# Kernel tuning notes

Hardware: AMD Instinct MI355X
Metric: run time of the kernel (lower is better)

Reference implementation:

```python
import jax, jax.numpy as jnp
import numpy as np

B, N, DIM, H = 2, 2048, 1024, 16
D = DIM // H  # head_dim = 64


def setup_inputs() -> dict:
    key = jax.random.key(0)
    ks = jax.random.split(key, 3)
    w_scale = 0.02
    return {
        "x": jax.random.normal(ks[0], (B, N, DIM), dtype=jnp.float32),
        "Wqkv": jax.random.normal(ks[1], (DIM, 3 * DIM), dtype=jnp.float32) * w_scale,
        "bqkv": jnp.zeros((3 * DIM,), dtype=jnp.float32),
        "Wproj": jax.random.normal(ks[2], (DIM, DIM), dtype=jnp.float32) * w_scale,
        "bproj": jnp.zeros((DIM,), dtype=jnp.float32),
        "sigma": jnp.ones((1,), dtype=jnp.float32),
        "gamma": jnp.ones((1,), dtype=jnp.float32),
    }


def reference(x, Wqkv, bqkv, Wproj, bproj, sigma, gamma):
    b, n, c = x.shape
    # qkv projection -> (B, N, 3, H, D)
    qkv = (x @ Wqkv + bqkv).reshape(b, n, 3, H, D)
    q = jnp.transpose(qkv[:, :, 0], (0, 2, 1, 3))  # [B, H, N, D]
    k = jnp.transpose(qkv[:, :, 1], (0, 2, 1, 3))
    v = jnp.transpose(qkv[:, :, 2], (0, 2, 1, 3))
    scale = 1.0 / jnp.sqrt(jnp.asarray(D, dtype=x.dtype))
    scores = jnp.einsum("bhqd,bhkd->bhqk", q, k) * scale  # [B, H, N, N]
    # divisive normalization (cortical gain control) over key axis
    denom = sigma + jnp.sqrt(jnp.mean(scores * scores, axis=-1, keepdims=True))
    scores = gamma * scores / denom
    attn = jax.nn.softmax(scores, axis=-1)
    out = jnp.einsum("bhqk,bhkd->bhqd", attn, v)  # [B, H, N, D]
    out = jnp.transpose(out, (0, 2, 1, 3)).reshape(b, n, c)
    return out @ Wproj + bproj
```

## Files before the change

kernel.cpp:

```cpp
#include <hip/hip_runtime.h>

typedef __attribute__((ext_vector_type(4))) float f32x4;
typedef __attribute__((ext_vector_type(8))) _Float16 f16x8;
typedef __attribute__((ext_vector_type(4))) _Float16 f16x4;
typedef __attribute__((ext_vector_type(2))) _Float16 f16x2;

#define MFMA_F16(a, b, c) __builtin_amdgcn_mfma_f32_16x16x32_f16(a, b, c, 0, 0, 0)

__device__ __forceinline__ void gload_lds16(const void* g, void* l) {
  __builtin_amdgcn_global_load_lds(
      (const __attribute__((address_space(1))) void*)g,
      (__attribute__((address_space(3))) void*)l, 16, 0, 0);
}
__device__ __forceinline__ f16x2 pk2(float a, float b) {
  return __builtin_bit_cast(f16x2, __builtin_amdgcn_cvt_pkrtz(a, b));
}
__device__ __forceinline__ void pipe_barrier_v4() {
  asm volatile("s_waitcnt vmcnt(4) lgkmcnt(0)" ::: "memory");
  __builtin_amdgcn_sched_barrier(0);
  __builtin_amdgcn_s_barrier();
}
__device__ __forceinline__ void pipe_barrier_v3() {
  asm volatile("s_waitcnt vmcnt(3) lgkmcnt(0)" ::: "memory");
  __builtin_amdgcn_sched_barrier(0);
  __builtin_amdgcn_s_barrier();
}
__device__ __forceinline__ void pipe_barrier_v2() {
  asm volatile("s_waitcnt vmcnt(2) lgkmcnt(0)" ::: "memory");
  __builtin_amdgcn_sched_barrier(0);
  __builtin_amdgcn_s_barrier();
}
__device__ __forceinline__ void pipe_barrier_v0() {
  asm volatile("s_waitcnt vmcnt(0) lgkmcnt(0)" ::: "memory");
  __builtin_amdgcn_sched_barrier(0);
  __builtin_amdgcn_s_barrier();
}

__global__ __launch_bounds__(256) void prep_kernel(
    const float* __restrict__ x, _Float16* __restrict__ xf,
    const float* __restrict__ Wqkv, _Float16* __restrict__ wqt,
    const float* __restrict__ Wproj, _Float16* __restrict__ wpt) {
  __shared__ float tile[32][33];
  const int bx = blockIdx.x;
  if (bx < 4096) {
    const int i = bx * 256 + threadIdx.x;
    f32x4 v = *(const f32x4*)(x + (size_t)i * 4);
    f16x4 h;
#pragma unroll
    for (int j = 0; j < 4; ++j) h[j] = (_Float16)v[j];
    *(f16x4*)(xf + (size_t)i * 4) = h;
    return;
  }
  const float* W;
  _Float16* wt;
  int N, n0, k0;
  if (bx < 7168) {
    const int t = bx - 4096;
    W = Wqkv; wt = wqt; N = 3072;
    n0 = (t % 96) * 32; k0 = (t / 96) * 32;
  } else {
    const int t = bx - 7168;
    W = Wproj; wt = wpt; N = 1024;
    n0 = (t % 32) * 32; k0 = (t / 32) * 32;
  }
  const int tx = threadIdx.x & 31, ty = threadIdx.x >> 5;
#pragma unroll
  for (int j = 0; j < 32; j += 8)
    tile[ty + j][tx] = W[(size_t)(k0 + ty + j) * N + n0 + tx];
  __syncthreads();
#pragma unroll
  for (int j = 0; j < 32; j += 8)
    wt[(size_t)(n0 + ty + j) * 1024 + k0 + tx] = (_Float16)tile[tx][ty + j];
}

__global__ __launch_bounds__(256) void gemm_qkv_kernel(
    const _Float16* __restrict__ xf, const _Float16* __restrict__ wt,
    const float* __restrict__ bias, _Float16* __restrict__ QF,
    _Float16* __restrict__ KF, _Float16* __restrict__ KT,
    _Float16* __restrict__ VT) {
  __shared__ __attribute__((aligned(16))) _Float16 lg[24576];
  const int tid = threadIdx.x, lane = tid & 63, w = tid >> 6;
  const int wg = blockIdx.x;
  const int cx = wg & 7, c = wg >> 3;
  const int bxl = (cx & 1) * 12 + c % 12;
  const int byl = (cx >> 1) * 8 + c / 12;
  const int m0 = byl * 128, n0 = bxl * 128;
  const int wr = (w >> 1) * 64, wc = (w & 1) * 64;
  f32x4 acc[4][4] = {};

  const int srow = lane >> 2;
  const int scol = (((lane & 3) ^ ((lane >> 3) & 3)) * 8);
  const int fr = lane & 15, fg = lane >> 4;
  const int rswz = (fr >> 1) & 3;

  auto stageT = [&](int buf, int k0) {
#pragma unroll
    for (int j = 0; j < 2; ++j) {
      const int rbase = 32 * w + 16 * j;
      const int r = rbase + srow;
      gload_lds16(xf + (size_t)(m0 + r) * 1024 + k0 + scol,
                  &lg[buf * 8192 + rbase * 32]);
      gload_lds16(wt + (size_t)(n0 + r) * 1024 + k0 + scol,
                  &lg[buf * 8192 + 4096 + rbase * 32]);
    }
  };
  auto mfma_step = [&](int ab) {
    f16x8 af[4], bfr[4];
#pragma unroll
    for (int m = 0; m < 4; ++m)
      af[m] = *(const f16x8*)&lg[ab + (wr + 16 * m + fr) * 32 + ((fg ^ rswz) * 8)];
#pragma unroll
    for (int n = 0; n < 4; ++n)
      bfr[n] = *(const f16x8*)&lg[ab + 4096 + (wc + 16 * n + fr) * 32 + ((fg ^ rswz) * 8)];
#pragma unroll
    for (int m = 0; m < 4; ++m)
#pragma unroll
      for (int n = 0; n < 4; ++n) acc[m][n] = MFMA_F16(af[m], bfr[n], acc[m][n]);
  };

  stageT(0, 0);
  stageT(1, 32);
  pipe_barrier_v4();
  for (int T = 0; T < 30; T += 3) {
#pragma unroll
    for (int s = 0; s < 3; ++s) {
      stageT((s + 2) % 3, (T + s + 2) * 32);
      mfma_step(s * 8192);
      pipe_barrier_v4();
    }
  }
  mfma_step(0);
  pipe_barrier_v0();
  mfma_step(8192);
  pipe_barrier_v0();

  const int fq = fg * 4;
#pragma unroll
  for (int n = 0; n < 4; ++n) {
    const float bv = bias[n0 + wc + 16 * n + fr];
#pragma unroll
    for (int m = 0; m < 4; ++m)
#pragma unroll
      for (int i = 0; i < 4; ++i)
        lg[(wr + 16 * m + fq + i) * 129 + wc + 16 * n + fr] =
            (_Float16)(acc[m][n][i] + bv);
  }
  __syncthreads();
  const int b = m0 >> 11, nnb = m0 & 2047;
  const int h0 = 2 * (bxl & 7);
  const int sPhase = bxl >> 3;
  if (sPhase <= 1) {
    _Float16* __restrict__ dst = (sPhase == 0) ? QF : KF;
#pragma unroll
    for (int p = 0; p < 8; ++p) {
      const int r = p * 16 + (tid >> 4);
      const int cc = tid & 15;
      f16x8 vals;
#pragma unroll
      for (int j = 0; j < 8; ++j) vals[j] = lg[r * 129 + cc * 8 + j];
      const int h = cc >> 3, d = (cc & 7) * 8;
      *(f16x8*)&dst[((size_t)((b * 16 + h0 + h) * 2048 + nnb + r)) * 64 + d] = vals;
    }
  }
  if (sPhase >= 1) {
    _Float16* __restrict__ T = (sPhase == 1) ? KT : VT;
#pragma unroll
    for (int p = 0; p < 8; ++p) {
      const int lr = p * 16 + (tid >> 4);
      const int cc = tid & 15;
      f16x8 vals;
#pragma unroll
      for (int j = 0; j < 8; ++j) vals[j] = lg[(cc * 8 + j) * 129 + lr];
      const int h = lr >> 6, d = lr & 63;
      *(f16x8*)&T[((size_t)((b * 16 + h0 + h) * 64 + d)) * 2048 + nnb + cc * 8] = vals;
    }
  }
}

__global__ __launch_bounds__(256) void gram_partial_kernel(
    const _Float16* __restrict__ KT, float* __restrict__ GP) {
  __shared__ __attribute__((aligned(16))) _Float16 sT[3][4096];
  const int tid = threadIdx.x, lane = tid & 63, w = tid >> 6;
  const int bh = blockIdx.x >> 2, qt = blockIdx.x & 3;
  const _Float16* src = KT + (size_t)bh * 64 * 2048 + qt * 512;
  const int s_r = lane >> 3, s_cg = lane & 7;
  const int fr = lane & 15, fg = lane >> 4;
  const int kswz = fr & 7;

  auto stage = [&](int buf, int n0) {
#pragma unroll
    for (int j = 0; j < 2; ++j) {
      const int rbase = 8 * w + 32 * j;
      gload_lds16(src + (size_t)(rbase + s_r) * 2048 + n0 + ((s_cg ^ s_r) * 8),
                  &sT[buf][rbase * 64]);
    }
  };

  f32x4 acc[4] = {};
  stage(0, 0);
  stage(1, 64);
  pipe_barrier_v2();
  int cur = 0;
#pragma unroll
  for (int t = 0; t < 8; ++t) {
    if (t < 6) {
      const int nb = (cur + 2 >= 3) ? cur - 1 : cur + 2;
      stage(nb, (t + 2) * 64);
    }
    f16x8 af[2];
#pragma unroll
    for (int ks = 0; ks < 2; ++ks)
      af[ks] = *(const f16x8*)&sT[cur][(16 * w + fr) * 64 + (((ks * 4 + fg) ^ kswz) * 8)];
#pragma unroll
    for (int nt = 0; nt < 4; ++nt)
#pragma unroll
      for (int ks = 0; ks < 2; ++ks)
        acc[nt] = MFMA_F16(
            af[ks],
            *(const f16x8*)&sT[cur][(16 * nt + fr) * 64 + (((ks * 4 + fg) ^ kswz) * 8)],
            acc[nt]);
    if (t < 6) pipe_barrier_v2(); else pipe_barrier_v0();
    cur = (cur + 1 == 3) ? 0 : cur + 1;
  }
  float* dst = GP + (size_t)blockIdx.x * 4096;
#pragma unroll
  for (int nt = 0; nt < 4; ++nt)
#pragma unroll
    for (int i = 0; i < 4; ++i)
      dst[(16 * w + fg * 4 + i) * 64 + 16 * nt + fr] = acc[nt][i];
}

__global__ __launch_bounds__(256) void gram_reduce_kernel(
    const float* __restrict__ GP, _Float16* __restrict__ GH,
    _Float16* __restrict__ GL) {
  const int bh = blockIdx.x >> 2, seg = blockIdx.x & 3;
  const int e0 = seg * 1024 + threadIdx.x * 4;
  const float* p = GP + (size_t)bh * 4 * 4096 + e0;
  f32x4 s = *(const f32x4*)p;
  s += *(const f32x4*)(p + 4096);
  s += *(const f32x4*)(p + 8192);
  s += *(const f32x4*)(p + 12288);
  f16x4 gh, gl;
#pragma unroll
  for (int j = 0; j < 4; ++j) {
    gh[j] = (_Float16)s[j];
    gl[j] = (_Float16)(s[j] - (float)gh[j]);
  }
  *(f16x4*)&GH[(size_t)bh * 4096 + e0] = gh;
  *(f16x4*)&GL[(size_t)bh * 4096 + e0] = gl;
}

__global__ __launch_bounds__(256) void attn_kernel(
    const _Float16* __restrict__ QF, const _Float16* __restrict__ KF,
    const _Float16* __restrict__ VT, const _Float16* __restrict__ GH,
    const _Float16* __restrict__ GL, _Float16* __restrict__ OB,
    const float* __restrict__ sigma_p, const float* __restrict__ gamma_p) {
  __shared__ __attribute__((aligned(16))) _Float16 lds[32768];

  const int tid = threadIdx.x, lane = tid & 63, w = tid >> 6;
  const int wg = blockIdx.x;
  const int c = wg >> 3;
  const int bh = (wg & 7) * 4 + (c >> 4);
  const int q0 = (c & 15) * 128;
  const size_t base = (size_t)bh * (2048 * 64);
  const float sigma = sigma_p[0], gamma = gamma_p[0];
  const int fr = lane & 15, fg = lane >> 4;
  const int s_r = lane >> 3, s_cg = lane & 7;
  const int kswz = fr & 7;

  const _Float16* Kbh = KF + base;
  const _Float16* Tbh = VT + base;

  f16x8 qf[2][2];
#pragma unroll
  for (int m = 0; m < 2; ++m)
#pragma unroll
    for (int ks = 0; ks < 2; ++ks)
      qf[m][ks] = *(const f16x8*)(QF + base +
                                  (size_t)(q0 + 32 * w + 16 * m + fr) * 64 +
                                  ks * 32 + fg * 8);

  auto stage64 = [&](int dstoff, const _Float16* g, int srcstride) {
#pragma unroll
    for (int j = 0; j < 2; ++j) {
      const int rbase = 8 * w + 32 * j;
      gload_lds16(g + (size_t)(rbase + s_r) * srcstride + ((s_cg ^ s_r) * 8),
                  &lds[dstoff + rbase * 64]);
    }
  };
  auto stage64K = [&](int dstoff, const _Float16* g) {
#pragma unroll
    for (int j = 0; j < 2; ++j) {
      const int rbase = 8 * w + 32 * j;
      const int r = rbase + s_r;
      const int pr = (r & 0x23) | ((r & 0x0C) << 1) | ((r & 0x10) >> 2);
      gload_lds16(g + (size_t)pr * 64 + ((s_cg ^ s_r) * 8),
                  &lds[dstoff + rbase * 64]);
    }
  };
  auto stage_tile = [&](int b, int kb) {
    stage64K(b * 4096, Kbh + (size_t)kb * 4096);
    stage64(16384 + b * 4096, Tbh + kb * 64, 2048);
  };

  stage64(0, GH + (size_t)bh * 4096, 64);
  stage64(4096, GL + (size_t)bh * 4096, 64);
  __syncthreads();
  float minvl2[2];
  float* Yp = (float*)&lds[8192 + w * 2048];
#pragma unroll
  for (int m = 0; m < 2; ++m) {
    f32x4 yacc[4] = {};
#pragma unroll
    for (int nt = 0; nt < 4; ++nt) {
#pragma unroll
      for (int ks = 0; ks < 2; ++ks) {
        const int off = (16 * nt + fr) * 64 + (((ks * 4 + fg) ^ kswz) * 8);
        yacc[nt] = MFMA_F16(qf[m][ks], *(const f16x8*)&lds[off], yacc[nt]);
        yacc[nt] = MFMA_F16(qf[m][ks], *(const f16x8*)&lds[4096 + off], yacc[nt]);
      }
    }
#pragma unroll
    for (int nt = 0; nt < 4; ++nt)
#pragma unroll
      for (int i = 0; i < 4; ++i) Yp[(fg * 4 + i) * 64 + 16 * nt + fr] = yacc[nt][i];
    float zp = 0.0f;
#pragma unroll
    for (int ks = 0; ks < 2; ++ks) {
      const f32x4 y0 = *(const f32x4*)&Yp[fr * 64 + ks * 32 + fg * 8];
      const f32x4 y1 = *(const f32x4*)&Yp[fr * 64 + ks * 32 + fg * 8 + 4];
#pragma unroll
      for (int cc = 0; cc < 4; ++cc) {
        zp += y0[cc] * (float)qf[m][ks][cc];
        zp += y1[cc] * (float)qf[m][ks][cc + 4];
      }
    }
    zp += __shfl_xor(zp, 16);
    zp += __shfl_xor(zp, 32);
    const float rms = sqrtf(fmaxf(zp, 0.0f)) * (1.0f / 362.038672f);
    minvl2[m] = gamma / (sigma + rms) * 0.125f * 1.44269504f;
  }
#pragma unroll
  for (int m = 0; m < 2; ++m)
#pragma unroll
    for (int ks = 0; ks < 2; ++ks) {
      f16x8 q = qf[m][ks], r;
#pragma unroll
      for (int j = 0; j < 4; ++j) {
        const f16x2 t = pk2((float)q[2 * j] * minvl2[m],
                            (float)q[2 * j + 1] * minvl2[m]);
        r[2 * j] = t[0];
        r[2 * j + 1] = t[1];
      }
      qf[m][ks] = r;
    }
  __syncthreads();

  f32x4 oacc[2][4] = {};
  f32x4 lacc[2] = {};
  f16x8 ones;
#pragma unroll
  for (int j = 0; j < 8; ++j) ones[j] = (_Float16)1.0f;

  auto qk_tile = [&](int kbuf, f32x4 (&pn)[2][4]) {
#pragma unroll
    for (int n = 0; n < 4; ++n) {
      const int offb = kbuf * 4096 + (16 * n + fr) * 64;
      const f16x8 kf0 = *(const f16x8*)&lds[offb + ((fg ^ kswz) * 8)];
      const f16x8 kf1 = *(const f16x8*)&lds[offb + (((4 + fg) ^ kswz) * 8)];
#pragma unroll
      for (int m = 0; m < 2; ++m) {
        f32x4 a = {};
        a = MFMA_F16(kf0, qf[m][0], a);
        a = MFMA_F16(kf1, qf[m][1], a);
        pn[m][n] = a;
      }
    }
  };
  auto exp_pack = [&](f32x4 (&pn)[2][4], f16x8 (&pa)[2][2]) {
#pragma unroll
    for (int m = 0; m < 2; ++m) {
#pragma unroll
      for (int n = 0; n < 4; ++n)
#pragma unroll
        for (int i = 0; i < 4; ++i)
          pn[m][n][i] = __builtin_amdgcn_exp2f(pn[m][n][i]);
#pragma unroll
      for (int k2 = 0; k2 < 2; ++k2) {
        const f16x2 c0 = pk2(pn[m][2 * k2][0], pn[m][2 * k2][1]);
        const f16x2 c1 = pk2(pn[m][2 * k2][2], pn[m][2 * k2][3]);
        const f16x2 c2 = pk2(pn[m][2 * k2 + 1][0], pn[m][2 * k2 + 1][1]);
        const f16x2 c3 = pk2(pn[m][2 * k2 + 1][2], pn[m][2 * k2 + 1][3]);
        pa[m][k2][0] = c0[0]; pa[m][k2][1] = c0[1];
        pa[m][k2][2] = c1[0]; pa[m][k2][3] = c1[1];
        pa[m][k2][4] = c2[0]; pa[m][k2][5] = c2[1];
        pa[m][k2][6] = c3[0]; pa[m][k2][7] = c3[1];
      }
    }
  };
  auto pv_tile = [&](int vbuf, f16x8 (&pa)[2][2]) {
#pragma unroll
    for (int k2 = 0; k2 < 2; ++k2) {
#pragma unroll
      for (int nf = 0; nf < 4; ++nf) {
        const int off = 16384 + vbuf * 4096 + (16 * nf + fr) * 64 +
                        (((k2 * 4 + fg) ^ kswz) * 8);
        const f16x8 vt = *(const f16x8*)&lds[off];
        oacc[0][nf] = MFMA_F16(vt, pa[0][k2], oacc[0][nf]);
        oacc[1][nf] = MFMA_F16(vt, pa[1][k2], oacc[1][nf]);
      }
      lacc[0] = MFMA_F16(ones, pa[0][k2], lacc[0]);
      lacc[1] = MFMA_F16(ones, pa[1][k2], lacc[1]);
    }
  };

  f32x4 pn[2][4];
  f16x8 pa[2][2][2];

  stage_tile(0, 0);
  stage_tile(1, 1);
  stage_tile(2, 2);
  pipe_barrier_v4();
  qk_tile(0, pn);
  exp_pack(pn, pa[0]);

  for (int T = 0; T < 28; T += 4) {
#pragma unroll
    for (int s = 0; s < 4; ++s) {
      stage_tile((s + 3) & 3, T + s + 3);
      __builtin_amdgcn_s_setprio(1);
      qk_tile((s + 1) & 3, pn);
      __builtin_amdgcn_s_setprio(0);
      __builtin_amdgcn_s_setprio(1);
      pv_tile(s & 3, pa[s & 1]);
      __builtin_amdgcn_s_setprio(0);
      exp_pack(pn, pa[(s + 1) & 1]);
      pipe_barrier_v4();
    }
  }
  {
    stage_tile(3, 31);
    __builtin_amdgcn_s_setprio(1); qk_tile(1, pn); __builtin_amdgcn_s_setprio(0);
    __builtin_amdgcn_s_setprio(1); pv_tile(0, pa[0]); __builtin_amdgcn_s_setprio(0);
    exp_pack(pn, pa[1]);
    pipe_barrier_v4();
    __builtin_amdgcn_s_setprio(1); qk_tile(2, pn); __builtin_amdgcn_s_setprio(0);
    __builtin_amdgcn_s_setprio(1); pv_tile(1, pa[1]); __builtin_amdgcn_s_setprio(0);
    exp_pack(pn, pa[0]);
    pipe_barrier_v0();
    __builtin_amdgcn_s_setprio(1); qk_tile(3, pn); __builtin_amdgcn_s_setprio(0);
    __builtin_amdgcn_s_setprio(1); pv_tile(2, pa[0]); __builtin_amdgcn_s_setprio(0);
    exp_pack(pn, pa[1]);
    pipe_barrier_v0();
    __builtin_amdgcn_s_setprio(1); pv_tile(3, pa[1]); __builtin_amdgcn_s_setprio(0);
  }

  float inv[2];
#pragma unroll
  for (int m = 0; m < 2; ++m) inv[m] = 1.0f / lacc[m][0];

  const int b = bh >> 4, h = bh & 15;
#pragma unroll
  for (int m = 0; m < 2; ++m) {
    const size_t orow = (size_t)(b * 2048 + q0 + 32 * w + 16 * m + fr);
#pragma unroll
    for (int nf = 0; nf < 4; ++nf) {
      f16x4 ov;
#pragma unroll
      for (int i = 0; i < 4; ++i) ov[i] = (_Float16)(oacc[m][nf][i] * inv[m]);
      *(f16x4*)&OB[orow * 1024 + h * 64 + 16 * nf + 4 * fg] = ov;
    }
  }
}

__global__ __launch_bounds__(256) void gemm_proj_kernel(
    const _Float16* __restrict__ A, const _Float16* __restrict__ Bt,
    const float* __restrict__ bias, float* __restrict__ out) {
  __shared__ __attribute__((aligned(16))) _Float16 lg[18432];
  const int tid = threadIdx.x, lane = tid & 63, w = tid >> 6;
  const int wg = blockIdx.x;
  const int c = wg >> 3;
  const int bxl = c & 7;
  const int byl = (wg & 7) * 8 + (c >> 3);
  const int m0 = byl * 64, n0 = bxl * 128;
  const int wr = (w >> 1) * 32, wc = (w & 1) * 64;
  f32x4 acc[2][4] = {};
  const int srow = lane >> 2;
  const int scol = (((lane & 3) ^ ((lane >> 3) & 3)) * 8);
  const int fr = lane & 15, fg = lane >> 4;
  const int rswz = (fr >> 1) & 3;

  auto stageT = [&](int buf, int k0) {
    {
      const int rbase = 16 * w;
      gload_lds16(A + (size_t)(m0 + rbase + srow) * 1024 + k0 + scol,
                  &lg[buf * 6144 + rbase * 32]);
    }
#pragma unroll
    for (int j = 0; j < 2; ++j) {
      const int rbase = 32 * w + 16 * j;
      gload_lds16(Bt + (size_t)(n0 + rbase + srow) * 1024 + k0 + scol,
                  &lg[buf * 6144 + 2048 + rbase * 32]);
    }
  };
  auto mfma_step = [&](int ab) {
    f16x8 af[2], bfr[4];
#pragma unroll
    for (int m = 0; m < 2; ++m)
      af[m] = *(const f16x8*)&lg[ab + (wr + 16 * m + fr) * 32 + ((fg ^ rswz) * 8)];
#pragma unroll
    for (int n = 0; n < 4; ++n)
      bfr[n] = *(const f16x8*)&lg[ab + 2048 + (wc + 16 * n + fr) * 32 + ((fg ^ rswz) * 8)];
#pragma unroll
    for (int m = 0; m < 2; ++m)
#pragma unroll
      for (int n = 0; n < 4; ++n) acc[m][n] = MFMA_F16(af[m], bfr[n], acc[m][n]);
  };

  stageT(0, 0);
  stageT(1, 32);
  pipe_barrier_v3();
  for (int T = 0; T < 30; T += 3) {
#pragma unroll
    for (int s = 0; s < 3; ++s) {
      stageT((s + 2) % 3, (T + s + 2) * 32);
      mfma_step(s * 6144);
      pipe_barrier_v3();
    }
  }
  mfma_step(0);
  pipe_barrier_v0();
  mfma_step(6144);
  pipe_barrier_v0();

  const int fq = fg * 4;
#pragma unroll
  for (int n = 0; n < 4; ++n) {
    const int col = n0 + wc + 16 * n + fr;
    const float bv = bias[col];
#pragma unroll
    for (int m = 0; m < 2; ++m) {
#pragma unroll
      for (int i = 0; i < 4; ++i) {
        const int row = m0 + wr + 16 * m + fq + i;
        out[(size_t)row * 1024 + col] = acc[m][n][i] + bv;
      }
    }
  }
}

extern "C" void kernel_launch(void* const* d_in, const int* in_sizes, int n_in,
                              void* d_out, int out_size, void* d_ws, size_t ws_size,
                              hipStream_t stream) {
  const float* x = (const float*)d_in[0];
  const float* Wqkv = (const float*)d_in[1];
  const float* bqkv = (const float*)d_in[2];
  const float* Wproj = (const float*)d_in[3];
  const float* bproj = (const float*)d_in[4];
  const float* sigma = (const float*)d_in[5];
  const float* gamma = (const float*)d_in[6];
  float* out = (float*)d_out;

  char* ws = (char*)d_ws;
  const size_t MB = 1024 * 1024;
  _Float16* XF  = (_Float16*)(ws + 0 * MB);
  _Float16* WQT = (_Float16*)(ws + 8 * MB);
  _Float16* WPT = (_Float16*)(ws + 14 * MB);
  _Float16* QF  = (_Float16*)(ws + 16 * MB);
  _Float16* KF  = (_Float16*)(ws + 24 * MB);
  _Float16* VT  = (_Float16*)(ws + 32 * MB);
  _Float16* KT  = (_Float16*)(ws + 40 * MB);
  _Float16* OB  = (_Float16*)(ws + 40 * MB);
  _Float16* GH  = (_Float16*)(ws + 8 * MB);
  _Float16* GL  = (_Float16*)(ws + 8 * MB + 512 * 1024);
  float*    GP  = (float*)(ws + 9 * MB);

  prep_kernel<<<8192, 256, 0, stream>>>(x, XF, Wqkv, WQT, Wproj, WPT);
  gemm_qkv_kernel<<<768, 256, 0, stream>>>(XF, WQT, bqkv, QF, KF, KT, VT);
  gram_partial_kernel<<<128, 256, 0, stream>>>(KT, GP);
  gram_reduce_kernel<<<128, 256, 0, stream>>>(GP, GH, GL);
  attn_kernel<<<512, 256, 0, stream>>>(QF, KF, VT, GH, GL, OB, sigma, gamma);
  gemm_proj_kernel<<<512, 256, 0, stream>>>(OB, WPT, bproj, out);
}
```

Measured before the change: 115.9 us.

## Fuse x fp16 conversion into QKV GEMM loads and split Gram partials finer

Removes the separate x-to-fp16 conversion pass: the QKV GEMM now loads fp32 x tiles into registers, converts them and writes them to LDS after the MFMA step, while weights still use direct global-to-LDS loads. This removes a full write and reread of the converted activations. The Gram partial kernel now splits the sequence into 8 chunks instead of 4 for more blocks, and the reduce kernel sums 8 partials. The trade-off is more registers and synchronous fp32 loads on the A path of the GEMM.

After: 140.8 us. 21.4% more time.

```diff
diff --git a/kernel.cpp b/kernel.cpp
--- a/kernel.cpp
+++ b/kernel.cpp
@@ -37,29 +37,18 @@
 }
 
 __global__ __launch_bounds__(256) void prep_kernel(
-    const float* __restrict__ x, _Float16* __restrict__ xf,
     const float* __restrict__ Wqkv, _Float16* __restrict__ wqt,
     const float* __restrict__ Wproj, _Float16* __restrict__ wpt) {
   __shared__ float tile[32][33];
   const int bx = blockIdx.x;
-  if (bx < 4096) {
-    const int i = bx * 256 + threadIdx.x;
-    f32x4 v = *(const f32x4*)(x + (size_t)i * 4);
-    f16x4 h;
-#pragma unroll
-    for (int j = 0; j < 4; ++j) h[j] = (_Float16)v[j];
-    *(f16x4*)(xf + (size_t)i * 4) = h;
-    return;
-  }
   const float* W;
   _Float16* wt;
   int N, n0, k0;
-  if (bx < 7168) {
-    const int t = bx - 4096;
+  if (bx < 3072) {
     W = Wqkv; wt = wqt; N = 3072;
-    n0 = (t % 96) * 32; k0 = (t / 96) * 32;
+    n0 = (bx % 96) * 32; k0 = (bx / 96) * 32;
   } else {
-    const int t = bx - 7168;
+    const int t = bx - 3072;
     W = Wproj; wt = wpt; N = 1024;
     n0 = (t % 32) * 32; k0 = (t / 32) * 32;
   }
@@ -74,7 +63,7 @@
 }
 
 __global__ __launch_bounds__(256) void gemm_qkv_kernel(
-    const _Float16* __restrict__ xf, const _Float16* __restrict__ wt,
+    const float* __restrict__ x, const _Float16* __restrict__ wt,
     const float* __restrict__ bias, _Float16* __restrict__ QF,
     _Float16* __restrict__ KF, _Float16* __restrict__ KT,
     _Float16* __restrict__ VT) {
@@ -93,13 +82,32 @@
   const int fr = lane & 15, fg = lane >> 4;
   const int rswz = (fr >> 1) & 3;
 
-  auto stageT = [&](int buf, int k0) {
+  auto a_load = [&](int k0, f32x4 (&ar)[4]) {
+#pragma unroll
+    for (int j = 0; j < 2; ++j) {
+      const int r = 32 * w + 16 * j + srow;
+      const float* src = x + (size_t)(m0 + r) * 1024 + k0 + scol;
+      ar[2 * j] = *(const f32x4*)src;
+      ar[2 * j + 1] = *(const f32x4*)(src + 4);
+    }
+  };
+  auto a_write = [&](int buf, const f32x4 (&ar)[4]) {
+#pragma unroll
+    for (int j = 0; j < 2; ++j) {
+      f16x8 h;
+#pragma unroll
+      for (int q = 0; q < 4; ++q) {
+        h[q] = (_Float16)ar[2 * j][q];
+        h[4 + q] = (_Float16)ar[2 * j + 1][q];
+      }
+      *(f16x8*)&lg[buf * 8192 + (32 * w + 16 * j) * 32 + lane * 8] = h;
+    }
+  };
+  auto b_stage = [&](int buf, int k0) {
 #pragma unroll
     for (int j = 0; j < 2; ++j) {
       const int rbase = 32 * w + 16 * j;
       const int r = rbase + srow;
-      gload_lds16(xf + (size_t)(m0 + r) * 1024 + k0 + scol,
-                  &lg[buf * 8192 + rbase * 32]);
       gload_lds16(wt + (size_t)(n0 + r) * 1024 + k0 + scol,
                   &lg[buf * 8192 + 4096 + rbase * 32]);
     }
@@ -118,15 +126,25 @@
       for (int n = 0; n < 4; ++n) acc[m][n] = MFMA_F16(af[m], bfr[n], acc[m][n]);
   };
 
-  stageT(0, 0);
-  stageT(1, 32);
-  pipe_barrier_v4();
+  {
+    f32x4 arA[4], arB[4];
+    a_load(0, arA);
+    b_stage(0, 0);
+    a_load(32, arB);
+    b_stage(1, 32);
+    a_write(0, arA);
+    a_write(1, arB);
+    pipe_barrier_v2();
+  }
   for (int T = 0; T < 30; T += 3) {
 #pragma unroll
     for (int s = 0; s < 3; ++s) {
-      stageT((s + 2) % 3, (T + s + 2) * 32);
+      f32x4 ar[4];
+      a_load((T + s + 2) * 32, ar);
+      b_stage((s + 2) % 3, (T + s + 2) * 32);
       mfma_step(s * 8192);
-      pipe_barrier_v4();
+      a_write((s + 2) % 3, ar);
+      pipe_barrier_v2();
     }
   }
   mfma_step(0);
@@ -181,8 +199,8 @@
     const _Float16* __restrict__ KT, float* __restrict__ GP) {
   __shared__ __attribute__((aligned(16))) _Float16 sT[3][4096];
   const int tid = threadIdx.x, lane = tid & 63, w = tid >> 6;
-  const int bh = blockIdx.x >> 2, qt = blockIdx.x & 3;
-  const _Float16* src = KT + (size_t)bh * 64 * 2048 + qt * 512;
+  const int bh = blockIdx.x >> 3, qt = blockIdx.x & 7;
+  const _Float16* src = KT + (size_t)bh * 64 * 2048 + qt * 256;
   const int s_r = lane >> 3, s_cg = lane & 7;
   const int fr = lane & 15, fg = lane >> 4;
   const int kswz = fr & 7;
@@ -195,33 +213,30 @@
                   &sT[buf][rbase * 64]);
     }
   };
-
   f32x4 acc[4] = {};
+  auto mm = [&](int buf) {
+    f16x8 af[2];
+#pragma unroll
+    for (int ks = 0; ks < 2; ++ks)
+      af[ks] = *(const f16x8*)&sT[buf][(16 * w + fr) * 64 + (((ks * 4 + fg) ^ kswz) * 8)];
+#pragma unroll
+    for (int nt = 0; nt < 4; ++nt)
+#pragma unroll
+      for (int ks = 0; ks < 2; ++ks)
+        acc[nt] = MFMA_F16(
+            af[ks],
+            *(const f16x8*)&sT[buf][(16 * nt + fr) * 64 + (((ks * 4 + fg) ^ kswz) * 8)],
+            acc[nt]);
+  };
+
   stage(0, 0);
   stage(1, 64);
   pipe_barrier_v2();
-  int cur = 0;
-#pragma unroll
-  for (int t = 0; t < 8; ++t) {
-    if (t < 6) {
-      const int nb = (cur + 2 >= 3) ? cur - 1 : cur + 2;
-      stage(nb, (t + 2) * 64);
-    }
-    f16x8 af[2];
-#pragma unroll
-    for (int ks = 0; ks < 2; ++ks)
-      af[ks] = *(const f16x8*)&sT[cur][(16 * w + fr) * 64 + (((ks * 4 + fg) ^ kswz) * 8)];
-#pragma unroll
-    for (int nt = 0; nt < 4; ++nt)
-#pragma unroll
-      for (int ks = 0; ks < 2; ++ks)
-        acc[nt] = MFMA_F16(
-            af[ks],
-            *(const f16x8*)&sT[cur][(16 * nt + fr) * 64 + (((ks * 4 + fg) ^ kswz) * 8)],
-            acc[nt]);
-    if (t < 6) pipe_barrier_v2(); else pipe_barrier_v0();
-    cur = (cur + 1 == 3) ? 0 : cur + 1;
-  }
+  stage(2, 128); mm(0); pipe_barrier_v2();
+  stage(0, 192); mm(1); pipe_barrier_v2();
+  mm(2); pipe_barrier_v0();
+  mm(0);
+
   float* dst = GP + (size_t)blockIdx.x * 4096;
 #pragma unroll
   for (int nt = 0; nt < 4; ++nt)
@@ -235,11 +250,10 @@
     _Float16* __restrict__ GL) {
   const int bh = blockIdx.x >> 2, seg = blockIdx.x & 3;
   const int e0 = seg * 1024 + threadIdx.x * 4;
-  const float* p = GP + (size_t)bh * 4 * 4096 + e0;
+  const float* p = GP + (size_t)bh * 8 * 4096 + e0;
   f32x4 s = *(const f32x4*)p;
-  s += *(const f32x4*)(p + 4096);
-  s += *(const f32x4*)(p + 8192);
-  s += *(const f32x4*)(p + 12288);
+#pragma unroll
+  for (int o = 1; o < 8; ++o) s += *(const f32x4*)(p + o * 4096);
   f16x4 gh, gl;
 #pragma unroll
   for (int j = 0; j < 4; ++j) {
@@ -563,7 +577,6 @@
 
   char* ws = (char*)d_ws;
   const size_t MB = 1024 * 1024;
-  _Float16* XF  = (_Float16*)(ws + 0 * MB);
   _Float16* WQT = (_Float16*)(ws + 8 * MB);
   _Float16* WPT = (_Float16*)(ws + 14 * MB);
   _Float16* QF  = (_Float16*)(ws + 16 * MB);
@@ -575,9 +588,9 @@
   _Float16* GL  = (_Float16*)(ws + 8 * MB + 512 * 1024);
   float*    GP  = (float*)(ws + 9 * MB);
 
-  prep_kernel<<<8192, 256, 0, stream>>>(x, XF, Wqkv, WQT, Wproj, WPT);
-  gemm_qkv_kernel<<<768, 256, 0, stream>>>(XF, WQT, bqkv, QF, KF, KT, VT);
-  gram_partial_kernel<<<128, 256, 0, stream>>>(KT, GP);
+  prep_kernel<<<4096, 256, 0, stream>>>(Wqkv, WQT, Wproj, WPT);
+  gemm_qkv_kernel<<<768, 256, 0, stream>>>(x, WQT, bqkv, QF, KF, KT, VT);
+  gram_partial_kernel<<<256, 256, 0, stream>>>(KT, GP);
   gram_reduce_kernel<<<128, 256, 0, stream>>>(GP, GH, GL);
   attn_kernel<<<512, 256, 0, stream>>>(QF, KF, VT, GH, GL, OB, sigma, gamma);
   gemm_proj_kernel<<<512, 256, 0, stream>>>(OB, WPT, bproj, out);
```
